# Kernel optimization log

Measured on AMD Instinct MI355X. Metric: run time of the kernel, lower is better.

The kernel has to match this reference:

```python
import jax, jax.numpy as jnp
import numpy as np

# Kronecker-sparse patterns (a,b,c,d), rightmost factor first, matching KSLinear.
PATTERNS = ((1, 64, 64, 64), (64, 64, 64, 1))
IN_SIZE = PATTERNS[0][0] * PATTERNS[0][2] * PATTERNS[0][3]   # 4096
OUT_SIZE = PATTERNS[-1][0] * PATTERNS[-1][1] * PATTERNS[-1][3]  # 4096
N_TOKENS = 16384


def setup_inputs() -> dict:
    key = jax.random.key(0)
    kx, k0, k1, kb = jax.random.split(key, 4)
    x = jax.random.normal(kx, (N_TOKENS, IN_SIZE), dtype=jnp.float32)
    # factors stored in native 4D (a,b,c,d) layout, uniform(-1/sqrt(c), 1/sqrt(c))
    a, b, c, d = PATTERNS[0]
    s0 = 1.0 / np.sqrt(c)
    f0 = jax.random.uniform(k0, (a, b, c, d), jnp.float32, -s0, s0)
    a, b, c, d = PATTERNS[1]
    s1 = 1.0 / np.sqrt(c)
    f1 = jax.random.uniform(k1, (a, b, c, d), jnp.float32, -s1, s1)
    bound = 1.0 / np.sqrt(IN_SIZE)
    bias = jax.random.uniform(kb, (OUT_SIZE,), jnp.float32, -bound, bound)
    return {"x": x, "f0": f0, "f1": f1, "bias": bias}


def _ks_apply(x, factor, pattern):
    # Apply one Kronecker-sparse factor with support I_a (x) 1_{b,c} (x) I_d.
    a, b, c, d = pattern
    batch = x.shape[:-1]
    x = x.reshape(*batch, a, c, d)                      # (..., a, c, d)
    y = jnp.einsum('...acd,abcd->...abd', x, factor)    # contract over c
    return y.reshape(*batch, a * b * d)


def reference(x, f0, f1, bias):
    y = _ks_apply(x, f0, PATTERNS[0])
    y = _ks_apply(y, f1, PATTERNS[1])
    return y + bias
```

## Files before the change

kernel.cpp:

```cpp
#include <hip/hip_runtime.h>
#include <cstdint>
#include <cstddef>

#define DI __device__ __forceinline__

using f32x4  = __attribute__((ext_vector_type(4))) float;
using bf16x8 = __attribute__((ext_vector_type(8))) short;
using u32x2  = __attribute__((ext_vector_type(2))) unsigned int;
using u32x4  = __attribute__((ext_vector_type(4))) unsigned int;

constexpr int NT = 16384;
constexpr int NF = 4096;

DI unsigned short f2bf(float f) {
  union { float f; unsigned u; } v; v.f = f;
  unsigned u = v.u;
  u += 0x7fffu + ((u >> 16) & 1u);
  return (unsigned short)(u >> 16);
}

DI void gload_lds16(const void* g, void* l) {
  __builtin_amdgcn_global_load_lds(
      (const __attribute__((address_space(1))) unsigned int*)g,
      (__attribute__((address_space(3))) unsigned int*)l, 16, 0, 0);
}

#define BAR_VM(N)                                              \
  do {                                                         \
    asm volatile("s_waitcnt vmcnt(" #N ")" ::: "memory");      \
    __builtin_amdgcn_s_barrier();                              \
    __builtin_amdgcn_sched_barrier(0);                         \
  } while (0)

__global__ void ks_prep(const float* __restrict__ f0, const float* __restrict__ f1,
                        unsigned short* __restrict__ f0s, unsigned short* __restrict__ f1s) {
  int tid = blockIdx.x * 256 + threadIdx.x;
  if (tid < 262144) {
    int d = tid & 63, c = (tid >> 6) & 63, b = tid >> 12;
    f0s[d * 4096 + b * 64 + c] = f2bf(f0[tid]);
  } else {
    int t2 = tid - 262144;
    f1s[t2] = f2bf(f1[t2]);
  }
}

__global__ __launch_bounds__(512, 4) void ks1(
    const float* __restrict__ x, const unsigned short* __restrict__ f0s,
    unsigned short* __restrict__ yp)
{
  __shared__ __align__(16) char L[32768 + 2 * 16640];
  char* const Xb0 = L;
  char* const Xb1 = L + 16384;
  char* const Yb0 = L + 32768;
  char* const Yb1 = L + 32768 + 16640;

  const int w  = blockIdx.x;
  const int tt = (w & 7) | ((w >> 6) << 3);
  const int dg = (w >> 3) & 7;
  const long T0 = (long)tt * 128;

  const int tid = threadIdx.x, lane = tid & 63, wv = tid >> 6;
  const int l15 = lane & 15, lq = lane >> 4;
  const int d = dg * 8 + wv;

  bf16x8 fA[4][2];
  #pragma unroll
  for (int bt = 0; bt < 4; ++bt)
    #pragma unroll
    for (int kh = 0; kh < 2; ++kh)
      fA[bt][kh] = *(const bf16x8*)(f0s + (size_t)d * 4096 + (bt * 16 + l15) * 64 + kh * 32 + lq * 8);

  const int st_t = tid >> 5, st_c0 = (tid >> 1) & 15, st_dq = tid & 1;
  const float* const xrow0 = x + (T0 + st_t) * (long)NF + dg * 8 + st_dq * 4;
  const int wkey = (st_t & 7) << 4;

  f32x4 r0, r1, r2, r3;
  auto issue = [&](int st) {
    const float* p = xrow0 + (long)st * 16 * NF + st_c0 * 4 * 64;
    r0 = *(const f32x4*)(p);
    r1 = *(const f32x4*)(p + 64);
    r2 = *(const f32x4*)(p + 128);
    r3 = *(const f32x4*)(p + 192);
  };
  auto stageX = [&](char* X) {
    #pragma unroll
    for (int e = 0; e < 4; ++e) {
      int p = st_dq * 4 + e;
      unsigned lo = (unsigned)f2bf(r0[e]) | ((unsigned)f2bf(r1[e]) << 16);
      unsigned hi = (unsigned)f2bf(r2[e]) | ((unsigned)f2bf(r3[e]) << 16);
      *(u32x2*)(X + p * 2048 + st_t * 128 + ((st_c0 * 8) ^ wkey)) = u32x2{lo, hi};
    }
  };

  issue(0);
  stageX(Xb0);
  issue(1);
  __syncthreads();

  const int rkey = (l15 & 7) << 4;

  for (int st = 0; st < 8; ++st) {
    char* const Xc = (st & 1) ? Xb1 : Xb0;
    char* const Xn = (st & 1) ? Xb0 : Xb1;
    char* const Yc = (st & 1) ? Yb1 : Yb0;

    const char* Xs = Xc + wv * 2048 + l15 * 128;
    bf16x8 bx0 = *(const bf16x8*)(Xs + ((0  + lq * 16) ^ rkey));
    bf16x8 bx1 = *(const bf16x8*)(Xs + ((64 + lq * 16) ^ rkey));
    f32x4 acc[4];
    #pragma unroll
    for (int bt = 0; bt < 4; ++bt) {
      acc[bt] = __builtin_amdgcn_mfma_f32_16x16x32_bf16(fA[bt][0], bx0, (f32x4){0.f,0.f,0.f,0.f}, 0, 0, 0);
      acc[bt] = __builtin_amdgcn_mfma_f32_16x16x32_bf16(fA[bt][1], bx1, acc[bt], 0, 0, 0);
    }

    {
      char* Yw = Yc + l15 * 1040 + wv * 2;
      #pragma unroll
      for (int bt = 0; bt < 4; ++bt)
        #pragma unroll
        for (int i = 0; i < 4; ++i)
          *(unsigned short*)(Yw + (bt * 16 + lq * 4 + i) * 16) = f2bf(acc[bt][i]);
    }

    stageX(Xn);
    issue(st + 2 <= 7 ? st + 2 : 7);
    __syncthreads();

    {
      const char* Yr = Yc;
      #pragma unroll
      for (int h = 0; h < 2; ++h) {
        int t = (tid >> 6) + h * 8;
        int c16 = tid & 63;
        u32x4 v = *(const u32x4*)(Yr + t * 1040 + c16 * 16);
        *(u32x4*)(yp + (T0 + st * 16 + t) * (size_t)NF + dg * 512 + c16 * 8) = v;
      }
    }
  }
}

__global__ __launch_bounds__(512, 4) void ks2(
    const unsigned short* __restrict__ yp, const unsigned short* __restrict__ f1s,
    const float* __restrict__ bias, float* __restrict__ out)
{
  __shared__ __align__(16) char Yb[4][16384];

  const int bid = blockIdx.x;
  const int ag  = bid & 7;
  const long T0 = (long)(bid >> 3) * 128;

  const int tid = threadIdx.x, lane = tid & 63, wv = tid >> 6;
  const int l15 = lane & 15, lq = lane >> 4;
  const int a = ag * 8 + wv;

  bf16x8 fa[4][2];
  #pragma unroll
  for (int bt = 0; bt < 4; ++bt)
    #pragma unroll
    for (int kh = 0; kh < 2; ++kh)
      fa[bt][kh] = *(const bf16x8*)(f1s + (size_t)a * 4096 + (bt * 16 + l15) * 64 + kh * 32 + lq * 8);
  f32x4 bv[4];
  #pragma unroll
  for (int bt = 0; bt < 4; ++bt)
    bv[bt] = *(const f32x4*)(bias + a * 64 + bt * 16 + lq * 4);

  auto stage = [&](int tile) {
    char* const dst = Yb[tile & 3];
    #pragma unroll
    for (int i = 0; i < 2; ++i) {
      const int trow = i * 8 + wv;
      const int g = lane ^ (trow & 7);
      const char* src = (const char*)yp + (T0 + (long)tile * 16 + trow) * 8192
                        + ((g >> 3) << 10) + ag * 128 + (g & 7) * 16;
      gload_lds16(src, dst + trow * 1024);
    }
  };

  stage(0); stage(1); stage(2);
  BAR_VM(4);

  #pragma unroll
  for (int j = 0; j < 8; ++j) {
    if (j + 3 < 8) stage(j + 3);

    const char* Yr = Yb[j & 3] + l15 * 1024;
    const int sw = wv ^ (l15 & 7);
    bf16x8 c0 = *(const bf16x8*)(Yr + ((lq * 8 + sw) * 16));
    bf16x8 c1 = *(const bf16x8*)(Yr + (((4 + lq) * 8 + sw) * 16));
    f32x4 acc[4];
    #pragma unroll
    for (int bt = 0; bt < 4; ++bt) {
      acc[bt] = __builtin_amdgcn_mfma_f32_16x16x32_bf16(fa[bt][0], c0, (f32x4){0.f,0.f,0.f,0.f}, 0, 0, 0);
      acc[bt] = __builtin_amdgcn_mfma_f32_16x16x32_bf16(fa[bt][1], c1, acc[bt], 0, 0, 0);
    }
    float* op = out + (T0 + (long)j * 16 + l15) * NF + a * 64 + lq * 4;
    #pragma unroll
    for (int bt = 0; bt < 4; ++bt)
      *(f32x4*)(op + bt * 16) = acc[bt] + bv[bt];

    switch (j) {
      case 0: BAR_VM(8);  break;
      case 1: BAR_VM(12); break;
      case 2: BAR_VM(16); break;
      case 3: BAR_VM(16); break;
      case 4: BAR_VM(16); break;
      case 5: BAR_VM(14); break;
      case 6: BAR_VM(12); break;
      default: break;
    }
  }
}

__global__ void ks_naive(const float* __restrict__ x, const float* __restrict__ f0,
                         const float* __restrict__ f1, const float* __restrict__ bias,
                         float* __restrict__ out)
{
  __shared__ float xr[4096];
  __shared__ float yr[4096];
  long t = blockIdx.x;
  int tid = threadIdx.x;
  for (int i = tid; i < 4096; i += 256) xr[i] = x[t * 4096 + i];
  __syncthreads();
  for (int i = tid; i < 4096; i += 256) {
    int b = i >> 6, d = i & 63;
    float s = 0.f;
    for (int c = 0; c < 64; ++c) s += xr[c * 64 + d] * f0[(b * 64 + c) * 64 + d];
    yr[i] = s;
  }
  __syncthreads();
  for (int i = tid; i < 4096; i += 256) {
    int a = i >> 6;
    float s = bias[i];
    for (int c = 0; c < 64; ++c) s += yr[a * 64 + c] * f1[(size_t)i * 64 + c];
    out[t * 4096 + i] = s;
  }
}

extern "C" void kernel_launch(void* const* d_in, const int* in_sizes, int n_in,
                              void* d_out, int out_size, void* d_ws, size_t ws_size,
                              hipStream_t stream) {
  const float* x    = (const float*)d_in[0];
  const float* f0   = (const float*)d_in[1];
  const float* f1   = (const float*)d_in[2];
  const float* bias = (const float*)d_in[3];
  float* out = (float*)d_out;

  const size_t ybytes = (size_t)NT * NF * 2;
  const size_t fbytes = (size_t)64 * 64 * 64 * 2;
  if (ws_size >= ybytes + 2 * fbytes) {
    unsigned short* yw  = (unsigned short*)d_ws;
    unsigned short* f0s = yw + (size_t)NT * NF;
    unsigned short* f1s = f0s + 64 * 64 * 64;
    ks_prep<<<2048, 256, 0, stream>>>(f0, f1, f0s, f1s);
    ks1<<<1024, 512, 0, stream>>>(x, f0s, yw);
    ks2<<<1024, 512, 0, stream>>>(yw, f1s, bias, out);
  } else {
    ks_naive<<<NT, 256, 0, stream>>>(x, f0, f1, bias, out);
  }
}
```

Measured before the change: 201.8 us.

## Deepen x prefetch in ks1 with dual register buffers and LDS-only barriers

The ks1 x-tile prefetch now uses two register buffers, so global loads run three stages ahead instead of two. The aim is to hide more of the latency of the fp32 input stream. Block barriers now wait only on lgkmcnt, so in-flight global loads no longer stall the barrier. The Y staging row pitch shrinks from 1040 to 1028 bytes to change the LDS bank mapping. That pitch leaves the 16-byte vector LDS reads unaligned, and the extra registers may press against the 4-blocks-per-SM launch bound.

New measurement: 211.4 us. +4.8%, slower.

```diff
diff --git a/kernel.cpp b/kernel.cpp
--- a/kernel.cpp
+++ b/kernel.cpp
@@ -25,6 +25,11 @@
       (__attribute__((address_space(3))) unsigned int*)l, 16, 0, 0);
 }
 
+DI void bar_lgkm() {
+  asm volatile("s_waitcnt lgkmcnt(0)" ::: "memory");
+  __builtin_amdgcn_s_barrier();
+  __builtin_amdgcn_sched_barrier(0);
+}
 #define BAR_VM(N)                                              \
   do {                                                         \
     asm volatile("s_waitcnt vmcnt(" #N ")" ::: "memory");      \
@@ -48,11 +53,11 @@
     const float* __restrict__ x, const unsigned short* __restrict__ f0s,
     unsigned short* __restrict__ yp)
 {
-  __shared__ __align__(16) char L[32768 + 2 * 16640];
+  __shared__ __align__(16) char L[32768 + 2 * 16448];
   char* const Xb0 = L;
   char* const Xb1 = L + 16384;
   char* const Yb0 = L + 32768;
-  char* const Yb1 = L + 32768 + 16640;
+  char* const Yb1 = L + 32768 + 16448;
 
   const int w  = blockIdx.x;
   const int tt = (w & 7) | ((w >> 6) << 3);
@@ -74,28 +79,29 @@
   const float* const xrow0 = x + (T0 + st_t) * (long)NF + dg * 8 + st_dq * 4;
   const int wkey = (st_t & 7) << 4;
 
-  f32x4 r0, r1, r2, r3;
-  auto issue = [&](int st) {
+  f32x4 rA[4], rB[4];
+  auto issueTo = [&](f32x4* r, int st) {
     const float* p = xrow0 + (long)st * 16 * NF + st_c0 * 4 * 64;
-    r0 = *(const f32x4*)(p);
-    r1 = *(const f32x4*)(p + 64);
-    r2 = *(const f32x4*)(p + 128);
-    r3 = *(const f32x4*)(p + 192);
+    r[0] = *(const f32x4*)(p);
+    r[1] = *(const f32x4*)(p + 64);
+    r[2] = *(const f32x4*)(p + 128);
+    r[3] = *(const f32x4*)(p + 192);
   };
-  auto stageX = [&](char* X) {
+  auto stageXFrom = [&](const f32x4* r, char* X) {
     #pragma unroll
     for (int e = 0; e < 4; ++e) {
       int p = st_dq * 4 + e;
-      unsigned lo = (unsigned)f2bf(r0[e]) | ((unsigned)f2bf(r1[e]) << 16);
-      unsigned hi = (unsigned)f2bf(r2[e]) | ((unsigned)f2bf(r3[e]) << 16);
+      unsigned lo = (unsigned)f2bf(r[0][e]) | ((unsigned)f2bf(r[1][e]) << 16);
+      unsigned hi = (unsigned)f2bf(r[2][e]) | ((unsigned)f2bf(r[3][e]) << 16);
       *(u32x2*)(X + p * 2048 + st_t * 128 + ((st_c0 * 8) ^ wkey)) = u32x2{lo, hi};
     }
   };
 
-  issue(0);
-  stageX(Xb0);
-  issue(1);
-  __syncthreads();
+  issueTo(rA, 0);
+  issueTo(rB, 1);
+  stageXFrom(rA, Xb0);
+  issueTo(rA, 2);
+  bar_lgkm();
 
   const int rkey = (l15 & 7) << 4;
 
@@ -115,7 +121,7 @@
     }
 
     {
-      char* Yw = Yc + l15 * 1040 + wv * 2;
+      char* Yw = Yc + l15 * 1028 + wv * 2;
       #pragma unroll
       for (int bt = 0; bt < 4; ++bt)
         #pragma unroll
@@ -123,9 +129,13 @@
           *(unsigned short*)(Yw + (bt * 16 + lq * 4 + i) * 16) = f2bf(acc[bt][i]);
     }
 
-    stageX(Xn);
-    issue(st + 2 <= 7 ? st + 2 : 7);
-    __syncthreads();
+    if (st < 7) {
+      f32x4* cons = (st & 1) ? rA : rB;
+      stageXFrom(cons, Xn);
+      if (st < 5) issueTo(cons, st + 3);
+    }
+
+    bar_lgkm();
 
     {
       const char* Yr = Yc;
@@ -133,7 +143,7 @@
       for (int h = 0; h < 2; ++h) {
         int t = (tid >> 6) + h * 8;
         int c16 = tid & 63;
-        u32x4 v = *(const u32x4*)(Yr + t * 1040 + c16 * 16);
+        u32x4 v = *(const u32x4*)(Yr + t * 1028 + c16 * 16);
         *(u32x4*)(yp + (T0 + st * 16 + t) * (size_t)NF + dg * 512 + c16 * 8) = v;
       }
     }
```

## Single-buffer ks1 Y staging, defer copy-out, raise occupancy with lgkm-only barriers

Applied to the files above, without the earlier changes.

Replaces the double-buffered Y tile in ks1's LDS with a single buffer. The copy-out of the previous sub-tile is deferred to the next iteration, and the Y row stride changes to 1028 bytes. LDS use drops, so launch bounds rise to 6 blocks per CU. __syncthreads is replaced by a barrier that waits only on lgkmcnt, so in-flight global loads are not drained, and redundant staging/issuing in the last iterations is skipped. The cost is an extra barrier per iteration, plus the risk of register pressure or spills from the higher occupancy target and the fully unrolled loop.

After: 243.5 us. +20.7%, slower.

```diff
diff --git a/kernel.cpp b/kernel.cpp
--- a/kernel.cpp
+++ b/kernel.cpp
@@ -25,6 +25,11 @@
       (__attribute__((address_space(3))) unsigned int*)l, 16, 0, 0);
 }
 
+DI void bar_lgkm() {
+  asm volatile("s_waitcnt lgkmcnt(0)" ::: "memory");
+  __builtin_amdgcn_s_barrier();
+  __builtin_amdgcn_sched_barrier(0);
+}
 #define BAR_VM(N)                                              \
   do {                                                         \
     asm volatile("s_waitcnt vmcnt(" #N ")" ::: "memory");      \
@@ -44,15 +49,14 @@
   }
 }
 
-__global__ __launch_bounds__(512, 4) void ks1(
+__global__ __launch_bounds__(512, 6) void ks1(
     const float* __restrict__ x, const unsigned short* __restrict__ f0s,
     unsigned short* __restrict__ yp)
 {
-  __shared__ __align__(16) char L[32768 + 2 * 16640];
+  __shared__ __align__(16) char L[32768 + 16448];
   char* const Xb0 = L;
   char* const Xb1 = L + 16384;
-  char* const Yb0 = L + 32768;
-  char* const Yb1 = L + 32768 + 16640;
+  char* const Yb  = L + 32768;
 
   const int w  = blockIdx.x;
   const int tt = (w & 7) | ((w >> 6) << 3);
@@ -91,18 +95,27 @@
       *(u32x2*)(X + p * 2048 + st_t * 128 + ((st_c0 * 8) ^ wkey)) = u32x2{lo, hi};
     }
   };
+  auto ycopy = [&](int sti) {
+    #pragma unroll
+    for (int h = 0; h < 2; ++h) {
+      int t = (tid >> 6) + h * 8;
+      int c16 = tid & 63;
+      u32x4 v = *(const u32x4*)(Yb + t * 1028 + c16 * 16);
+      *(u32x4*)(yp + (T0 + sti * 16 + t) * (size_t)NF + dg * 512 + c16 * 8) = v;
+    }
+  };
 
   issue(0);
   stageX(Xb0);
   issue(1);
-  __syncthreads();
+  bar_lgkm();
 
   const int rkey = (l15 & 7) << 4;
 
+  #pragma unroll
   for (int st = 0; st < 8; ++st) {
-    char* const Xc = (st & 1) ? Xb1 : Xb0;
+    const char* const Xc = (st & 1) ? Xb1 : Xb0;
     char* const Xn = (st & 1) ? Xb0 : Xb1;
-    char* const Yc = (st & 1) ? Yb1 : Yb0;
 
     const char* Xs = Xc + wv * 2048 + l15 * 128;
     bf16x8 bx0 = *(const bf16x8*)(Xs + ((0  + lq * 16) ^ rkey));
@@ -114,8 +127,15 @@
       acc[bt] = __builtin_amdgcn_mfma_f32_16x16x32_bf16(fA[bt][1], bx1, acc[bt], 0, 0, 0);
     }
 
+    if (st > 0) ycopy(st - 1);
+
+    if (st < 7) stageX(Xn);
+    if (st < 6) issue(st + 2);
+
+    bar_lgkm();
+
     {
-      char* Yw = Yc + l15 * 1040 + wv * 2;
+      char* Yw = Yb + l15 * 1028 + wv * 2;
       #pragma unroll
       for (int bt = 0; bt < 4; ++bt)
         #pragma unroll
@@ -123,21 +143,10 @@
           *(unsigned short*)(Yw + (bt * 16 + lq * 4 + i) * 16) = f2bf(acc[bt][i]);
     }
 
-    stageX(Xn);
-    issue(st + 2 <= 7 ? st + 2 : 7);
-    __syncthreads();
-
-    {
-      const char* Yr = Yc;
-      #pragma unroll
-      for (int h = 0; h < 2; ++h) {
-        int t = (tid >> 6) + h * 8;
-        int c16 = tid & 63;
-        u32x4 v = *(const u32x4*)(Yr + t * 1040 + c16 * 16);
-        *(u32x4*)(yp + (T0 + st * 16 + t) * (size_t)NF + dg * 512 + c16 * 8) = v;
-      }
-    }
-  }
+    bar_lgkm();
+  }
+
+  ycopy(7);
 }
 
 __global__ __launch_bounds__(512, 4) void ks2(
```
